# Performance work log

Hardware: AMD Instinct MI355X
Metric: run time of the kernel (lower is better)

## Reference

```python
import jax, jax.numpy as jnp
import numpy as np

B, L, C = 8, 999, 768
C2 = C // 2           # 384 per branch
H, HD = 8, C2 // 8    # heads, head_dim=48
K, G = 3, 2           # dynamic conv kernel size, num_groups
DC_IN = C2 // 4       # DynamicConv1d proj inner (reduction_ratio default 4) = 96
PJ_IN = max(16, C // 8)  # mixer proj inner_dim = 96
SCALE = HD ** -0.5
EPS = 1e-5


def _gelu(x):
    return jax.nn.gelu(x, approximate=False)


def _c1x1(x, w, b):
    # pointwise conv1d: x (B,Cin,L), w (Cout,Cin), b (Cout,)
    return jnp.einsum('bcl,oc->bol', x, w) + b[None, :, None]


def _dw3(x, w, b):
    # depthwise conv1d k=3 pad=1: x (B,Ch,L), w (Ch,3), b (Ch,) or None
    Lx = x.shape[-1]
    xp = jnp.pad(x, ((0, 0), (0, 0), (1, 1)))
    y = (xp[:, :, 0:Lx] * w[:, 0][None, :, None]
         + xp[:, :, 1:Lx + 1] * w[:, 1][None, :, None]
         + xp[:, :, 2:Lx + 2] * w[:, 2][None, :, None])
    if b is not None:
        y = y + b[None, :, None]
    return y


def _bn(x, g, b):
    # BatchNorm1d, training-mode batch stats over (B, L): x (B,Ch,L)
    m = x.mean(axis=(0, 2), keepdims=True)
    v = ((x - m) ** 2).mean(axis=(0, 2), keepdims=True)
    return (x - m) * jax.lax.rsqrt(v + EPS) * g[None, :, None] + b[None, :, None]


def setup_inputs() -> dict:
    key = jax.random.key(0)
    ks = jax.random.split(key, 30)
    s = 0.02
    d = {
        'x': jax.random.normal(ks[0], (B, L, C), jnp.float32),
        # DynamicConv1d (dim=384, K=3, G=2, inner=96)
        'dc_weight': jax.random.normal(ks[1], (G, C2, K), jnp.float32) * s,
        'dc_bias':   jax.random.normal(ks[2], (G, C2), jnp.float32) * s,
        'dc_p1w':    jax.random.normal(ks[3], (DC_IN, C2), jnp.float32) * s,
        'dc_p1b':    jax.random.normal(ks[4], (DC_IN,), jnp.float32) * s,
        'dc_p2w':    jax.random.normal(ks[5], (C2 * G, DC_IN), jnp.float32) * s,
        'dc_p2b':    jax.random.normal(ks[6], (C2 * G,), jnp.float32) * s,
        # Attention (dim=384, heads=8, sr_ratio=1 -> sr=Identity)
        'at_qw':  jax.random.normal(ks[7], (C2, C2), jnp.float32) * s,
        'at_qb':  jax.random.normal(ks[8], (C2,), jnp.float32) * s,
        'at_kvw': jax.random.normal(ks[9], (2 * C2, C2), jnp.float32) * s,
        'at_kvb': jax.random.normal(ks[10], (2 * C2,), jnp.float32) * s,
        'at_lcw': jax.random.normal(ks[11], (C2, K), jnp.float32) * s,
        'at_lcb': jax.random.normal(ks[12], (C2,), jnp.float32) * s,
        # mixer proj
        'pj_dww':  jax.random.normal(ks[13], (C, K), jnp.float32) * s,
        'pj_dwb':  jax.random.normal(ks[14], (C,), jnp.float32) * s,
        'pj_bn1g': jnp.ones((C,), jnp.float32),
        'pj_bn1b': jnp.zeros((C,), jnp.float32),
        'pj_c1w':  jax.random.normal(ks[15], (PJ_IN, C), jnp.float32) * s,
        'pj_c1b':  jax.random.normal(ks[16], (PJ_IN,), jnp.float32) * s,
        'pj_bn2g': jnp.ones((PJ_IN,), jnp.float32),
        'pj_bn2b': jnp.zeros((PJ_IN,), jnp.float32),
        'pj_c2w':  jax.random.normal(ks[17], (C, PJ_IN), jnp.float32) * s,
        'pj_c2b':  jax.random.normal(ks[18], (C,), jnp.float32) * s,
        'pj_bn3g': jnp.ones((C,), jnp.float32),
        'pj_bn3b': jnp.zeros((C,), jnp.float32),
    }
    return d


def _dynamic_conv(x, dc_weight, dc_bias, p1w, p1b, p2w, p2b):
    # x: (B, L, C2)
    xt = jnp.transpose(x, (0, 2, 1))                 # (B,C2,L)
    # AdaptiveAvgPool1d(K) with L divisible by K -> exact non-overlapping mean
    pooled = xt.reshape(B, C2, K, L // K).mean(-1)   # (B,C2,K)
    sc = _c1x1(_gelu(_c1x1(pooled, p1w, p1b)), p2w, p2b)  # (B, G*C2, K)
    sc = jax.nn.softmax(sc.reshape(B, G, C2, K), axis=1)
    w = (sc * dc_weight[None]).sum(axis=1)           # (B,C2,K) per-sample kernels
    xm = xt.mean(axis=2, keepdims=True)              # (B,C2,1)
    sb = _c1x1(_gelu(_c1x1(xm, p1w, p1b)), p2w, p2b) # (B, G*C2, 1)
    sb = jax.nn.softmax(sb.reshape(B, G, C2), axis=1)
    bias = (sb * dc_bias[None]).sum(axis=1)          # (B,C2)
    # depthwise per-(b,c) conv, k=3, pad=1
    xp = jnp.pad(xt, ((0, 0), (0, 0), (1, 1)))
    y = (xp[:, :, 0:L] * w[:, :, 0:1]
         + xp[:, :, 1:L + 1] * w[:, :, 1:2]
         + xp[:, :, 2:L + 2] * w[:, :, 2:3]) + bias[:, :, None]
    return jnp.transpose(y, (0, 2, 1))               # (B,L,C2)


def _attention(x, qw, qb, kvw, kvb, lcw, lcb):
    # x: (B, L, C2)
    xt = jnp.transpose(x, (0, 2, 1))                 # (B,C2,L)
    q = _c1x1(xt, qw, qb).reshape(B, H, HD, L)
    q = jnp.transpose(q, (0, 1, 3, 2))               # (B,H,L,HD)
    kv_in = _dw3(xt, lcw, lcb) + xt                  # local_conv(kv)+kv (sr=Identity)
    kv = _c1x1(kv_in, kvw, kvb)                      # (B,2*C2,L)
    k = kv[:, :C2].reshape(B, H, HD, L)              # (B,H,HD,L)
    v = jnp.transpose(kv[:, C2:].reshape(B, H, HD, L), (0, 1, 3, 2))  # (B,H,L,HD)
    attn = jnp.einsum('bhld,bhdm->bhlm', q, k) * SCALE
    attn = jax.nn.softmax(attn, axis=-1)
    out = jnp.einsum('bhlm,bhmd->bhld', attn, v)     # (B,H,L,HD)
    # faithful to torch: transpose(-1,-2) then reshape(B, L, C2)
    out = jnp.transpose(out, (0, 1, 3, 2)).reshape(B, L, C2)
    return out


def reference(x, dc_weight, dc_bias, dc_p1w, dc_p1b, dc_p2w, dc_p2b,
              at_qw, at_qb, at_kvw, at_kvb, at_lcw, at_lcb,
              pj_dww, pj_dwb, pj_bn1g, pj_bn1b, pj_c1w, pj_c1b,
              pj_bn2g, pj_bn2b, pj_c2w, pj_c2b, pj_bn3g, pj_bn3b):
    x1 = x[:, :, :C2]
    x2 = x[:, :, C2:]
    x1 = _dynamic_conv(x1, dc_weight, dc_bias, dc_p1w, dc_p1b, dc_p2w, dc_p2b)
    x2 = _attention(x2, at_qw, at_qb, at_kvw, at_kvb, at_lcw, at_lcb)
    xc = jnp.concatenate([x1, x2], axis=2)           # (B,L,C)
    xt = jnp.transpose(xc, (0, 2, 1))                # (B,C,L)
    h = _bn(_gelu(_dw3(xt, pj_dww, pj_dwb)), pj_bn1g, pj_bn1b)
    h = _bn(_gelu(_c1x1(h, pj_c1w, pj_c1b)), pj_bn2g, pj_bn2b)
    h = _bn(_c1x1(h, pj_c2w, pj_c2b), pj_bn3g, pj_bn3b)
    out = h + xt
    return jnp.transpose(out, (0, 2, 1))             # (B,L,C)
```

## Files before the change

kernel.cpp:

```cpp
#include <hip/hip_runtime.h>
#include <cstddef>

constexpr int B = 8, L = 999, C = 768, C2 = 384, H = 8, HD = 48;
constexpr int KVL = 1000;
constexpr float ATT_SCALE = 0.14433756729740644f;
constexpr float LOG2E = 1.4426950408889634f;
constexpr float BN_EPS = 1e-5f;
constexpr float INV_N = 1.0f / (8.0f * 999.0f);

constexpr size_t SZ_XT   = (size_t)B * C * L;
constexpr size_t SZ_HALF = (size_t)B * C2 * L;
constexpr size_t OFF_XT  = 0;
constexpr size_t OFF_XT2 = SZ_XT;
constexpr size_t OFF_KV  = 2 * SZ_XT;
constexpr size_t OFF_AX  = 3 * SZ_XT;
constexpr size_t OFF_Q   = 3 * SZ_XT + SZ_HALF;
constexpr size_t OFF_SM  = 3 * SZ_XT + SZ_HALF + SZ_HALF / 2;

constexpr size_t SM_POOLED = 0;
constexpr size_t SM_XM     = 9216;
constexpr size_t SM_H1     = 12288;
constexpr size_t SM_WDYN   = 15360;
constexpr size_t SM_BDYN   = 24576;
constexpr size_t SM_SUM1   = 27648;
constexpr size_t SM_SQ1    = 28416;
constexpr size_t SM_CB1    = 30720;
constexpr size_t SM_SUM2   = 30816;
constexpr size_t SM_SQ2    = 30912;
constexpr size_t SM_CB2    = 31200;
constexpr size_t SM_SUM3   = 31968;
constexpr size_t SM_SQ3    = 32736;
constexpr size_t SM_ZEND   = 33504;
constexpr size_t SM_END    = 35040;
constexpr size_t SM_WQ  = SM_END;
constexpr size_t SM_WKV = SM_WQ + 73728;
constexpr size_t SM_WC1 = SM_WKV + 147456;
constexpr size_t SM_WC2 = SM_WC1 + 36864;

typedef __attribute__((ext_vector_type(8))) short bf16x8;
typedef __attribute__((ext_vector_type(4))) float floatx4;

__device__ __forceinline__ float gelu_f(float x) {
  return 0.5f * x * (1.0f + erff(x * 0.70710678118654752f));
}

__device__ __forceinline__ float wave_sum(float v) {
  #pragma unroll
  for (int off = 32; off > 0; off >>= 1) v += __shfl_down(v, off, 64);
  return v;
}

__device__ __forceinline__ short f2bf(float f) {
  union { float f; unsigned u; } x; x.f = f;
  unsigned r = x.u + 0x7FFFu + ((x.u >> 16) & 1u);
  return (short)(r >> 16);
}

__device__ __forceinline__ bf16x8 pack8(const float* p) {
  union { unsigned u[4]; bf16x8 v; } r;
  asm("v_cvt_pk_bf16_f32 %0, %1, %2" : "=v"(r.u[0]) : "v"(p[0]), "v"(p[1]));
  asm("v_cvt_pk_bf16_f32 %0, %1, %2" : "=v"(r.u[1]) : "v"(p[2]), "v"(p[3]));
  asm("v_cvt_pk_bf16_f32 %0, %1, %2" : "=v"(r.u[2]) : "v"(p[4]), "v"(p[5]));
  asm("v_cvt_pk_bf16_f32 %0, %1, %2" : "=v"(r.u[3]) : "v"(p[6]), "v"(p[7]));
  return r.v;
}

__device__ __forceinline__ float exp2_hw(float x) {
  float r;
  asm("v_exp_f32 %0, %1" : "=v"(r) : "v"(x));
  return r;
}

#define BNA(x, su, qq, gg) { float m_ = (su) * INV_N; float v_ = (qq) * INV_N - m_ * m_; \
  float sc_ = (gg) * rsqrtf(v_ + BN_EPS); (x) = ((x) - m_) * sc_; }

__global__ void k_pre_t(const float* __restrict__ qw, short* __restrict__ wq,
                        const float* __restrict__ kvw, short* __restrict__ wkv,
                        const float* __restrict__ c1w, short* __restrict__ wc1,
                        const float* __restrict__ c2w, short* __restrict__ wc2,
                        const float* __restrict__ c1b, const float* __restrict__ bn1b,
                        const float* __restrict__ c2b, const float* __restrict__ bn2b,
                        float* __restrict__ cb1, float* __restrict__ cb2,
                        const float* __restrict__ x, float* __restrict__ xt) {
  __shared__ float tile[32][33];
  int bid = blockIdx.x;
  int t = threadIdx.y * 32 + threadIdx.x;
  if (bid < 288) {
    const float* src; short* dst; int base;
    if (bid < 72)       { src = qw;  dst = wq;  base = bid; }
    else if (bid < 216) { src = kvw; dst = wkv; base = bid - 72; }
    else if (bid < 252) { src = c1w; dst = wc1; base = bid - 216; }
    else                { src = c2w; dst = wc2; base = bid - 252; }
    int i = (base * 256 + t) * 8;
    float4 a = *reinterpret_cast<const float4*>(&src[i]);
    float4 b = *reinterpret_cast<const float4*>(&src[i + 4]);
    short tmp[8] = {f2bf(a.x), f2bf(a.y), f2bf(a.z), f2bf(a.w),
                    f2bf(b.x), f2bf(b.y), f2bf(b.z), f2bf(b.w)};
    *(bf16x8*)&dst[i] = *(bf16x8*)tmp;
  } else if (bid == 288) {
    if (t < 96) {
      float a = c1b[t];
      const float* wr = c1w + (size_t)t * C;
      for (int c = 0; c < C; c++) a += bn1b[c] * wr[c];
      cb1[t] = a;
    }
  } else if (bid == 289) {
    for (int o = t; o < C; o += 256) {
      float a = c2b[o];
      const float* wr = c2w + (size_t)o * 96;
      for (int i = 0; i < 96; i++) a += bn2b[i] * wr[i];
      cb2[o] = a;
    }
  } else {
    int tb = bid - 290;
    int bx = tb % 32, by = (tb / 32) % 12, bz = tb / 384;
    int l0 = bx * 32, c0 = by * 32;
    int tx = threadIdx.x, ty = threadIdx.y;
    #pragma unroll
    for (int i = 0; i < 4; i++) {
      int l = l0 + ty + i * 8, c = c0 + tx;
      if (l < L) tile[ty + i * 8][tx] = x[((size_t)bz * L + l) * C + c];
    }
    __syncthreads();
    #pragma unroll
    for (int i = 0; i < 4; i++) {
      int c = c0 + ty + i * 8, l = l0 + tx;
      if (l < L) xt[((size_t)bz * C + c) * L + l] = tile[tx][ty + i * 8];
    }
  }
}

__global__ __launch_bounds__(384) void k_kvin(const float* __restrict__ x,
                                              const float* __restrict__ lcw,
                                              const float* __restrict__ lcb,
                                              short* __restrict__ x2bf,
                                              short* __restrict__ kvinbf) {
  int b = blockIdx.y, l0 = blockIdx.x * 8, c = threadIdx.x;
  float w0 = lcw[c * 3], w1 = lcw[c * 3 + 1] + 1.0f, w2 = lcw[c * 3 + 2], bb = lcb[c];
  const float* xb = x + (size_t)b * L * C + C2 + c;
  float prev = (l0 > 0) ? xb[(size_t)(l0 - 1) * C] : 0.f;
  float cur  = (l0 < L) ? xb[(size_t)l0 * C] : 0.f;
  #pragma unroll
  for (int r = 0; r < 8; r++) {
    int l = l0 + r;
    if (l >= L) break;
    float nxt = (l + 1 < L) ? xb[(size_t)(l + 1) * C] : 0.f;
    x2bf[((size_t)b * L + l) * C2 + c]   = f2bf(cur);
    kvinbf[((size_t)b * L + l) * C2 + c] = f2bf(prev * w0 + cur * w1 + nxt * w2 + bb);
    prev = cur; cur = nxt;
  }
}

__global__ __launch_bounds__(256) void k_pool(const float* __restrict__ xt,
                                              float* __restrict__ pooled,
                                              float* __restrict__ xm) {
  int c = blockIdx.x, b = blockIdx.y;
  const float* row = xt + ((size_t)b * C + c) * L;
  float s0 = 0.f, s1 = 0.f, s2 = 0.f;
  for (int l = threadIdx.x; l < L; l += 256) {
    float v = row[l];
    int ch = l / 333;
    if (ch == 0) s0 += v; else if (ch == 1) s1 += v; else s2 += v;
  }
  s0 = wave_sum(s0); s1 = wave_sum(s1); s2 = wave_sum(s2);
  __shared__ float r[3][4];
  int lane = threadIdx.x & 63, wid = threadIdx.x >> 6;
  if (lane == 0) { r[0][wid] = s0; r[1][wid] = s1; r[2][wid] = s2; }
  __syncthreads();
  if (threadIdx.x == 0) {
    float t0 = r[0][0] + r[0][1] + r[0][2] + r[0][3];
    float t1 = r[1][0] + r[1][1] + r[1][2] + r[1][3];
    float t2 = r[2][0] + r[2][1] + r[2][2] + r[2][3];
    size_t pb = (size_t)(b * C2 + c) * 3;
    pooled[pb + 0] = t0 / 333.f;
    pooled[pb + 1] = t1 / 333.f;
    pooled[pb + 2] = t2 / 333.f;
    xm[b * C2 + c] = (t0 + t1 + t2) / 999.f;
  }
}

__global__ void k_mlp1(const float* __restrict__ pooled, const float* __restrict__ xm,
                       const float* __restrict__ p1w, const float* __restrict__ p1b,
                       float* __restrict__ h1) {
  int j = blockIdx.x, b = blockIdx.y;
  __shared__ float vin[C2];
  for (int c = threadIdx.x; c < C2; c += 128)
    vin[c] = (j < 3) ? pooled[(size_t)(b * C2 + c) * 3 + j] : xm[b * C2 + c];
  __syncthreads();
  int o = threadIdx.x;
  if (o < 96) {
    float acc = p1b[o];
    const float* wr = p1w + (size_t)o * C2;
    for (int c = 0; c < C2; c++) acc += vin[c] * wr[c];
    h1[(b * 4 + j) * 96 + o] = gelu_f(acc);
  }
}

__global__ void k_mix2(const float* __restrict__ h1,
                       const float* __restrict__ p2w, const float* __restrict__ p2b,
                       const float* __restrict__ dcw, const float* __restrict__ dcb,
                       float* __restrict__ wdyn, float* __restrict__ bdyn) {
  int j = blockIdx.x, b = blockIdx.y;
  __shared__ float hv[96];
  for (int i = threadIdx.x; i < 96; i += 384) hv[i] = h1[(b * 4 + j) * 96 + i];
  __syncthreads();
  int c = threadIdx.x;
  float a0 = p2b[c], a1 = p2b[C2 + c];
  const float* w0r = p2w + (size_t)c * 96;
  const float* w1r = p2w + (size_t)(C2 + c) * 96;
  for (int i = 0; i < 96; i++) { float h = hv[i]; a0 += h * w0r[i]; a1 += h * w1r[i]; }
  float m = fmaxf(a0, a1);
  float e0 = __expf(a0 - m), e1 = __expf(a1 - m);
  float inv = 1.f / (e0 + e1);
  float p0 = e0 * inv, p1 = e1 * inv;
  if (j < 3)
    wdyn[(size_t)(b * C2 + c) * 3 + j] = p0 * dcw[(size_t)c * 3 + j] + p1 * dcw[(size_t)(C2 + c) * 3 + j];
  else
    bdyn[b * C2 + c] = p0 * dcb[c] + p1 * dcb[C2 + c];
}

__global__ __launch_bounds__(256) void k_dwconv(const float* __restrict__ xt,
                                                const float* __restrict__ wdyn,
                                                const float* __restrict__ bdyn,
                                                float* __restrict__ xt2) {
  int c = blockIdx.x, b = blockIdx.y;
  const float* rowA = xt + ((size_t)b * C + c) * L;
  size_t wb = (size_t)(b * C2 + c) * 3;
  float a0 = wdyn[wb], a1 = wdyn[wb + 1], a2 = wdyn[wb + 2], ab = bdyn[b * C2 + c];
  float* oA = xt2 + ((size_t)b * C + c) * L;
  for (int l = threadIdx.x; l < L; l += 256) {
    float xm1 = (l > 0) ? rowA[l - 1] : 0.f;
    float x0 = rowA[l];
    float xp1 = (l < L - 1) ? rowA[l + 1] : 0.f;
    oA[l] = xm1 * a0 + x0 * a1 + xp1 * a2 + ab;
  }
}

template<int LT, bool XBF16>
__device__ __forceinline__ void gemm_body(const short* __restrict__ Wbf,
                                          const void* __restrict__ Xv,
                                          void* __restrict__ Yv,
                                          const float* __restrict__ ssum,
                                          const float* __restrict__ ssq,
                                          const float* __restrict__ sg,
                                          const float* __restrict__ bias,
                                          float* __restrict__ osum, float* __restrict__ osq,
                                          int O, int Kd, int Kstride, int XLd, int Ldy,
                                          size_t xbs, size_t ybs,
                                          int flags, float outmul,
                                          int kc, size_t slice,
                                          int o0, int l0, int b,
                                          short* Xt) {
  constexpr int R = LT / 32;
  constexpr int XSZ = LT * 72;
  int kbeg = kc * Kd;
  int t = threadIdx.x, w = t >> 6, lane = t & 63;
  int col = lane & 15, quad = lane >> 4;
  int KT = (Kd + 63) >> 6;

  floatx4 acc[LT / 16];
  #pragma unroll
  for (int i = 0; i < LT / 16; i++) acc[i] = floatx4{0.f, 0.f, 0.f, 0.f};

  int orow = o0 + w * 16 + col;
  bool wok = orow < O;
  const short* Wrow = Wbf + (size_t)orow * Kstride + kbeg;

  const short* Xb16 = (const short*)Xv + (size_t)b * xbs + kbeg;
  const float* Xb32 = (const float*)Xv + (size_t)b * xbs + kbeg;

  bf16x8 xr[R];
  float4 xf[R][2];
  bf16x8 wcur0, wcur1, wnxt0, wnxt1;

  auto xload = [&](int k0) {
    #pragma unroll
    for (int r = 0; r < R; r++) {
      int u = t + r * 256;
      int ll = u >> 3, oct = u & 7;
      int l = l0 + ll, kk = k0 + oct * 8;
      bool ok = (l < L) && (kk < Kd);
      if constexpr (XBF16) {
        xr[r] = ok ? *(const bf16x8*)&Xb16[(size_t)l * XLd + kk]
                   : bf16x8{0, 0, 0, 0, 0, 0, 0, 0};
      } else {
        if (ok) {
          const float* p = &Xb32[(size_t)l * XLd + kk];
          float4 a = *(const float4*)p;
          float4 bq = *(const float4*)(p + 4);
          if (sg) {
            float4 u0 = *(const float4*)&ssum[kbeg + kk];
            float4 u1 = *(const float4*)&ssum[kbeg + kk + 4];
            float4 q0 = *(const float4*)&ssq[kbeg + kk];
            float4 q1 = *(const float4*)&ssq[kbeg + kk + 4];
            float4 g0 = *(const float4*)&sg[kbeg + kk];
            float4 g1 = *(const float4*)&sg[kbeg + kk + 4];
            BNA(a.x, u0.x, q0.x, g0.x);  BNA(a.y, u0.y, q0.y, g0.y);
            BNA(a.z, u0.z, q0.z, g0.z);  BNA(a.w, u0.w, q0.w, g0.w);
            BNA(bq.x, u1.x, q1.x, g1.x); BNA(bq.y, u1.y, q1.y, g1.y);
            BNA(bq.z, u1.z, q1.z, g1.z); BNA(bq.w, u1.w, q1.w, g1.w);
          }
          xf[r][0] = a;
          xf[r][1] = bq;
        } else {
          xf[r][0] = float4{0.f, 0.f, 0.f, 0.f};
          xf[r][1] = float4{0.f, 0.f, 0.f, 0.f};
        }
      }
    }
  };
  auto xwrite = [&](int buf) {
    #pragma unroll
    for (int r = 0; r < R; r++) {
      int u = t + r * 256;
      int ll = u >> 3, oct = u & 7;
      bf16x8 val;
      if constexpr (XBF16) {
        val = xr[r];
      } else {
        union { unsigned u4[4]; bf16x8 v; } pk;
        asm("v_cvt_pk_bf16_f32 %0, %1, %2" : "=v"(pk.u4[0]) : "v"(xf[r][0].x), "v"(xf[r][0].y));
        asm("v_cvt_pk_bf16_f32 %0, %1, %2" : "=v"(pk.u4[1]) : "v"(xf[r][0].z), "v"(xf[r][0].w));
        asm("v_cvt_pk_bf16_f32 %0, %1, %2" : "=v"(pk.u4[2]) : "v"(xf[r][1].x), "v"(xf[r][1].y));
        asm("v_cvt_pk_bf16_f32 %0, %1, %2" : "=v"(pk.u4[3]) : "v"(xf[r][1].z), "v"(xf[r][1].w));
        val = pk.v;
      }
      *(bf16x8*)&Xt[buf * XSZ + ll * 72 + oct * 8] = val;
    }
  };
  auto wload = [&](int k0, bf16x8& f0, bf16x8& f1) {
    int kk0 = k0 + quad * 8;
    int kk1 = k0 + 32 + quad * 8;
    f0 = (wok && kk0 < Kd) ? *(const bf16x8*)&Wrow[kk0] : bf16x8{0, 0, 0, 0, 0, 0, 0, 0};
    f1 = (wok && kk1 < Kd) ? *(const bf16x8*)&Wrow[kk1] : bf16x8{0, 0, 0, 0, 0, 0, 0, 0};
  };

  xload(0);
  wload(0, wcur0, wcur1);
  xwrite(0);
  __syncthreads();

  for (int it = 0; it < KT; ++it) {
    int curb = it & 1;
    bool more = (it + 1 < KT);
    if (more) { xload((it + 1) * 64); wload((it + 1) * 64, wnxt0, wnxt1); }
    #pragma unroll
    for (int nt = 0; nt < LT / 16; nt++) {
      bf16x8 bx0 = *(bf16x8*)&Xt[curb * XSZ + (nt * 16 + col) * 72 + quad * 8];
      acc[nt] = __builtin_amdgcn_mfma_f32_16x16x32_bf16(wcur0, bx0, acc[nt], 0, 0, 0);
      bf16x8 bx1 = *(bf16x8*)&Xt[curb * XSZ + (nt * 16 + col) * 72 + 32 + quad * 8];
      acc[nt] = __builtin_amdgcn_mfma_f32_16x16x32_bf16(wcur1, bx1, acc[nt], 0, 0, 0);
    }
    if (more) xwrite(curb ^ 1);
    __syncthreads();
    wcur0 = wnxt0; wcur1 = wnxt1;
  }

  int o_base = o0 + w * 16 + quad * 4;
  #pragma unroll
  for (int r = 0; r < 4; r++) {
    int o = o_base + r;
    bool ov = o < O;
    float bo = (bias && ov) ? bias[o] : 0.f;
    float ps = 0.f, pq = 0.f;
    #pragma unroll
    for (int nt = 0; nt < LT / 16; nt++) {
      int l = l0 + nt * 16 + col;
      float v = acc[nt][r] + bo;
      if (flags & 1) v = gelu_f(v);
      v *= outmul;
      if (l >= L) v = 0.f;
      if (ov && l < L) {
        if (flags & 2) ((short*)Yv)[(size_t)b * ybs + (size_t)o * Ldy + l] = f2bf(v);
        else           ((float*)Yv)[kc * slice + (size_t)b * ybs + (size_t)o * Ldy + l] = v;
      }
      ps += v; pq += v * v;
    }
    if ((flags & 8) && ov) {
      ps += __shfl_xor(ps, 1); ps += __shfl_xor(ps, 2);
      ps += __shfl_xor(ps, 4); ps += __shfl_xor(ps, 8);
      pq += __shfl_xor(pq, 1); pq += __shfl_xor(pq, 2);
      pq += __shfl_xor(pq, 4); pq += __shfl_xor(pq, 8);
      if (col == 0) { atomicAdd(&osum[o], ps); atomicAdd(&osq[o], pq); }
    }
  }
}

template<int LT, bool XBF16>
__global__ __launch_bounds__(256) void k_gemm3(const short* __restrict__ Wbf,
                                               const void* __restrict__ Xv,
                                               void* __restrict__ Yv,
                                               const float* __restrict__ ssum,
                                               const float* __restrict__ ssq,
                                               const float* __restrict__ sg,
                                               const float* __restrict__ bias,
                                               float* __restrict__ osum, float* __restrict__ osq,
                                               int O, int Kd, int Kstride, int XLd, int Ldy,
                                               size_t xbs, size_t ybs,
                                               int flags, float outmul,
                                               int ksplit, size_t slice) {
  __shared__ __align__(16) short Xt[2][LT * 72];
  int kc = (int)blockIdx.y % ksplit;
  int o0 = ((int)blockIdx.y / ksplit) * 64;
  gemm_body<LT, XBF16>(Wbf, Xv, Yv, ssum, ssq, sg, bias, osum, osq,
                       O, Kd, Kstride, XLd, Ldy, xbs, ybs, flags, outmul,
                       kc, slice, o0, blockIdx.x * LT, blockIdx.z, &Xt[0][0]);
}

__global__ __launch_bounds__(256) void k_gemm_qkv(const short* __restrict__ wq,
                                                  const short* __restrict__ wkv,
                                                  const short* __restrict__ x2,
                                                  const short* __restrict__ kvin,
                                                  short* __restrict__ qout,
                                                  short* __restrict__ kvout,
                                                  const float* __restrict__ qbias,
                                                  const float* __restrict__ kvbias) {
  __shared__ __align__(16) short Xt[2][128 * 72];
  int y = blockIdx.y;
  if (y < 6) {
    gemm_body<128, true>(wq, (const void*)x2, (void*)qout,
                         nullptr, nullptr, nullptr, qbias, nullptr, nullptr,
                         C2, C2, C2, C2, L, (size_t)C2 * L, (size_t)C2 * L,
                         2, ATT_SCALE * LOG2E, 0, 0,
                         y * 64, blockIdx.x * 128, blockIdx.z, &Xt[0][0]);
  } else {
    gemm_body<128, true>(wkv, (const void*)kvin, (void*)kvout,
                         nullptr, nullptr, nullptr, kvbias, nullptr, nullptr,
                         C, C2, C2, C2, KVL, (size_t)C2 * L, (size_t)C * KVL,
                         2, 1.0f, 0, 0,
                         (y - 6) * 64, blockIdx.x * 128, blockIdx.z, &Xt[0][0]);
  }
}

__global__ __launch_bounds__(256) void k_h2fin_t(const float* __restrict__ part,
                                                 const float* __restrict__ cb1,
                                                 float* __restrict__ h2,
                                                 float* __restrict__ sum, float* __restrict__ sq) {
  __shared__ float tile[96][33];
  __shared__ float lsum[96], lsq[96];
  constexpr size_t SL = (size_t)B * 96 * L;
  int b = blockIdx.y, l0 = blockIdx.x * 32;
  int t = threadIdx.x;
  #pragma unroll
  for (int p = 0; p < 12; p++) {
    int u = t + p * 256;
    int o = u >> 5, li = u & 31;
    int l = l0 + li;
    float v = 0.f;
    if (l < L) {
      size_t idx = ((size_t)b * 96 + o) * L + l;
      v = gelu_f(part[idx] + part[SL + idx] + part[2 * SL + idx] + part[3 * SL + idx] + cb1[o]);
    }
    tile[o][li] = v;
    float vs = v, vq = v * v;
    vs += __shfl_xor(vs, 1); vs += __shfl_xor(vs, 2); vs += __shfl_xor(vs, 4);
    vs += __shfl_xor(vs, 8); vs += __shfl_xor(vs, 16);
    vq += __shfl_xor(vq, 1); vq += __shfl_xor(vq, 2); vq += __shfl_xor(vq, 4);
    vq += __shfl_xor(vq, 8); vq += __shfl_xor(vq, 16);
    if ((t & 31) == 0) { lsum[o] = vs; lsq[o] = vq; }
  }
  __syncthreads();
  if (t < 96) { atomicAdd(&sum[t], lsum[t]); atomicAdd(&sq[t], lsq[t]); }
  #pragma unroll
  for (int p = 0; p < 12; p++) {
    int u = t + p * 256;
    int lr = u / 96, o = u % 96;
    int l = l0 + lr;
    if (l < L) h2[((size_t)b * L + l) * 96 + o] = tile[o][lr];
  }
}

__global__ __launch_bounds__(512, 4) void k_attn_mfma(const short* __restrict__ q,
                                                      const short* __restrict__ kv,
                                                      float* __restrict__ out) {
  __shared__ __align__(16) char smem[2 * 8192 + 2 * 6144 + 33280];
  short* Ks0 = (short*)smem;
  short* Ks1 = (short*)(smem + 8192);
  short* Vf0 = (short*)(smem + 16384);
  short* Vf1 = (short*)(smem + 22528);
  float* PF  = (float*)(smem + 28672);
  float* Os  = (float*)smem;

  int lt0 = blockIdx.x * 128;
  int h = blockIdx.y, b = blockIdx.z;
  int t = threadIdx.x;
  int w = t >> 6, lane = t & 63;
  int col = lane & 15, quad = lane >> 4;
  const short* qb = q  + ((size_t)b * C2 + h * HD) * L;
  const short* kb = kv + ((size_t)b * C  + h * HD) * KVL;
  const short* vb = kv + ((size_t)b * C + C2 + h * HD) * KVL;

  bf16x8 aq0, aq1;
  {
    int l = lt0 + w * 16 + col;
    bool ok = l < L;
    const short* qp = qb + (size_t)(quad * 8) * L + l;
    short v0[8];
    #pragma unroll
    for (int jj = 0; jj < 8; jj++) v0[jj] = ok ? qp[(size_t)jj * L] : (short)0;
    aq0 = *(bf16x8*)v0;
    if (quad < 2) {
      const short* qp1 = qb + (size_t)(32 + quad * 8) * L + l;
      short v1[8];
      #pragma unroll
      for (int jj = 0; jj < 8; jj++) v1[jj] = ok ? qp1[(size_t)jj * L] : (short)0;
      aq1 = *(bf16x8*)v1;
    } else {
      aq1 = bf16x8{0, 0, 0, 0, 0, 0, 0, 0};
    }
  }

  short kreg[8];
  bf16x8 vreg;

  auto stage_load = [&](int m0) {
    if (t < 384) {
      int m = t & 63, j = t >> 6;
      int gm = m0 + m;
      bool ok = gm < L;
      const short* src = kb + (size_t)(8 * j) * KVL + gm;
      #pragma unroll
      for (int jj = 0; jj < 8; jj++) kreg[jj] = ok ? src[(size_t)jj * KVL] : (short)0;
    }
    if (t >= 128) {
      int a = t - 128;
      int d = (a & 7) | ((a >> 6) << 3);
      int o = (a >> 3) & 7;
      int mb = m0 + o * 8;
      const short* src = vb + (size_t)d * KVL + mb;
      if (mb + 8 <= L) {
        vreg = *(const bf16x8*)src;
      } else {
        short tmp[8];
        #pragma unroll
        for (int j = 0; j < 8; j++) tmp[j] = (mb + j < L) ? src[j] : (short)0;
        vreg = *(bf16x8*)tmp;
      }
    }
  };
  auto stage_write = [&](short* Kd, short* Vd) {
    if (t < 384) {
      int m = t & 63, j = t >> 6;
      int slot = ((m >> 4) * 2 + (j >> 2)) * 64 + (j & 3) * 16 + (m & 15);
      *(bf16x8*)&Kd[slot * 8] = *(bf16x8*)kreg;
    }
    if (t >= 128) {
      int a = t - 128;
      int d = (a & 7) | ((a >> 6) << 3);
      int o = (a >> 3) & 7;
      int lanep = ((o & 3) << 4) | (d & 15);
      *(bf16x8*)&Vd[(((o >> 2) * 3 + (d >> 4)) * 64 + lanep) * 8] = vreg;
    }
  };

  if (t < 256) {
    int i = t & 127;
    int ms = i >> 5, qq = 2 + ((i >> 4) & 1), cc = i & 15;
    int slot = (ms * 2 + 1) * 64 + qq * 16 + cc;
    short* Kd = (t < 128) ? Ks0 : Ks1;
    *(bf16x8*)&Kd[slot * 8] = bf16x8{0, 0, 0, 0, 0, 0, 0, 0};
  }

  stage_load(0);
  stage_write(Ks0, Vf0);

  floatx4 of[3];
  #pragma unroll
  for (int i = 0; i < 3; i++) of[i] = floatx4{0.f, 0.f, 0.f, 0.f};
  float rs[4] = {0.f, 0.f, 0.f, 0.f};
  __syncthreads();

  for (int it = 0; it < 16; ++it) {
    int m0 = it * 64;
    short* Kc = (it & 1) ? Ks1 : Ks0;
    short* Vc = (it & 1) ? Vf1 : Vf0;
    short* Kn = (it & 1) ? Ks0 : Ks1;
    short* Vn = (it & 1) ? Vf0 : Vf1;
    if (it < 15) stage_load(m0 + 64);

    floatx4 sf[4];
    __builtin_amdgcn_s_setprio(1);
    #pragma unroll
    for (int ms = 0; ms < 4; ms++) {
      bf16x8 bk0 = *(bf16x8*)&Kc[((ms * 2 + 0) * 64 + lane) * 8];
      bf16x8 bk1 = *(bf16x8*)&Kc[((ms * 2 + 1) * 64 + lane) * 8];
      floatx4 a4 = floatx4{0.f, 0.f, 0.f, 0.f};
      a4 = __builtin_amdgcn_mfma_f32_16x16x32_bf16(aq0, bk0, a4, 0, 0, 0);
      a4 = __builtin_amdgcn_mfma_f32_16x16x32_bf16(aq1, bk1, a4, 0, 0, 0);
      sf[ms] = a4;
    }
    __builtin_amdgcn_s_setprio(0);

    float* pw = PF + w * 1040 + lane;
    #pragma unroll
    for (int ms = 0; ms < 4; ms++) {
      int m = m0 + ms * 16 + col;
      bool ok = m < L;
      #pragma unroll
      for (int r = 0; r < 4; r++) {
        float e = ok ? exp2_hw(sf[ms][r]) : 0.f;
        rs[r] += e;
        pw[(ms * 4 + r) * 65] = e;
      }
    }

    const float* pr = PF + w * 1040 + (col & 3) * 65 + (col >> 2) * 16 + (quad & 1) * 8;
    __builtin_amdgcn_s_setprio(1);
    #pragma unroll
    for (int mh = 0; mh < 2; mh++) {
      const float* ps = pr + (mh * 2 + (quad >> 1)) * 260;
      float p8[8];
      #pragma unroll
      for (int jj = 0; jj < 8; jj++) p8[jj] = ps[jj];
      bf16x8 ap = pack8(p8);
      #pragma unroll
      for (int ds = 0; ds < 3; ds++) {
        bf16x8 bv = *(bf16x8*)&Vc[((mh * 3 + ds) * 64 + lane) * 8];
        of[ds] = __builtin_amdgcn_mfma_f32_16x16x32_bf16(ap, bv, of[ds], 0, 0, 0);
      }
    }
    __builtin_amdgcn_s_setprio(0);
    if (it < 15) stage_write(Kn, Vn);
    __syncthreads();
  }

  #pragma unroll
  for (int r = 0; r < 4; r++) {
    float v = rs[r];
    v += __shfl_xor(v, 1); v += __shfl_xor(v, 2);
    v += __shfl_xor(v, 4); v += __shfl_xor(v, 8);
    rs[r] = v;
  }
  #pragma unroll
  for (int r = 0; r < 4; r++) {
    float inv = 1.f / rs[r];
    #pragma unroll
    for (int ds = 0; ds < 3; ds++)
      Os[(ds * 16 + col) * 130 + w * 16 + quad * 4 + r] = of[ds][r] * inv;
  }
  __syncthreads();
  for (int i = t; i < 48 * 128; i += 512) {
    int d = i >> 7, ll = i & 127;
    int l = lt0 + ll;
    if (l < L) out[((size_t)b * C2 + h * HD + d) * L + l] = Os[d * 130 + ll];
  }
}

__global__ __launch_bounds__(256) void k_dwproj_t(const float* __restrict__ xt2,
                                                  const float* __restrict__ ao,
                                                  const float* __restrict__ dww,
                                                  const float* __restrict__ dwb,
                                                  float* __restrict__ t1,
                                                  float* __restrict__ sum, float* __restrict__ sq) {
  __shared__ float tile[32][67];
  __shared__ float rs[4][32], rq[4][32];
  int b = blockIdx.z, c0 = blockIdx.y * 32, l0 = blockIdx.x * 64;
  int t = threadIdx.x;
  if (c0 < C2) {
    for (int u = t; u < 32 * 66; u += 256) {
      int cc = u / 66, li = u % 66;
      int l = l0 - 1 + li;
      tile[cc][li] = (l >= 0 && l < L) ? xt2[((size_t)b * C + c0 + cc) * L + l] : 0.f;
    }
  } else {
    for (int u = t; u < 32 * 66; u += 256) {
      int li = u >> 5, cc = u & 31;
      int l = l0 - 1 + li;
      tile[cc][li] = (l >= 0 && l < L) ? ao[((size_t)b * L + l) * C2 + (c0 - C2 + cc)] : 0.f;
    }
  }
  __syncthreads();
  int c = c0 + (t & 31);
  float w0 = dww[c * 3], w1 = dww[c * 3 + 1], w2 = dww[c * 3 + 2], bb = dwb[c];
  int cc = t & 31;
  float s = 0.f, s2 = 0.f;
  #pragma unroll
  for (int p = 0; p < 8; p++) {
    int lr = (t >> 5) + p * 8;
    int l = l0 + lr;
    float v = 0.f;
    if (l < L) {
      v = gelu_f(tile[cc][lr] * w0 + tile[cc][lr + 1] * w1 + tile[cc][lr + 2] * w2 + bb);
      t1[((size_t)b * L + l) * C + c] = v;
    }
    s += v; s2 += v * v;
  }
  s += __shfl_xor(s, 32, 64); s2 += __shfl_xor(s2, 32, 64);
  int wv = t >> 6, ln = t & 63;
  if (ln < 32) { rs[wv][ln] = s; rq[wv][ln] = s2; }
  __syncthreads();
  if (t < 32) {
    float a = rs[0][t] + rs[1][t] + rs[2][t] + rs[3][t];
    float qq = rq[0][t] + rq[1][t] + rq[2][t] + rq[3][t];
    atomicAdd(&sum[c0 + t], a);
    atomicAdd(&sq[c0 + t], qq);
  }
}

__global__ void k_final(const float* __restrict__ y3, const float* __restrict__ xt2,
                        const float* __restrict__ ao,
                        const float* __restrict__ sum3, const float* __restrict__ sq3,
                        const float* __restrict__ bn3g, const float* __restrict__ bn3b,
                        float* __restrict__ out) {
  __shared__ float tile[32][33];
  int b = blockIdx.z;
  int l0 = blockIdx.x * 32, c0 = blockIdx.y * 32;
  int tx = threadIdx.x, ty = threadIdx.y;
  #pragma unroll
  for (int i = 0; i < 4; i++) {
    int c = c0 + ty + i * 8, l = l0 + tx;
    if (l < L) {
      float m = sum3[c] * INV_N;
      float v = sq3[c] * INV_N - m * m;
      float sc = bn3g[c] * rsqrtf(v + BN_EPS);
      float dd = bn3b[c] - m * sc;
      size_t idx = ((size_t)b * C + c) * L + l;
      float val = y3[idx] * sc + dd;
      if (c < C2) val += xt2[idx];
      tile[ty + i * 8][tx] = val;
    }
  }
  __syncthreads();
  #pragma unroll
  for (int i = 0; i < 4; i++) {
    int l = l0 + ty + i * 8, c = c0 + tx;
    if (l < L) {
      float val = tile[tx][ty + i * 8];
      if (c >= C2) val += ao[((size_t)b * L + l) * C2 + (c - C2)];
      out[((size_t)b * L + l) * C + c] = val;
    }
  }
}

extern "C" void kernel_launch(void* const* d_in, const int* in_sizes, int n_in,
                              void* d_out, int out_size, void* d_ws, size_t ws_size,
                              hipStream_t stream) {
  const float* x    = (const float*)d_in[0];
  const float* dcw  = (const float*)d_in[1];
  const float* dcb  = (const float*)d_in[2];
  const float* p1w  = (const float*)d_in[3];
  const float* p1b  = (const float*)d_in[4];
  const float* p2w  = (const float*)d_in[5];
  const float* p2b  = (const float*)d_in[6];
  const float* qw   = (const float*)d_in[7];
  const float* qb   = (const float*)d_in[8];
  const float* kvw  = (const float*)d_in[9];
  const float* kvb  = (const float*)d_in[10];
  const float* lcw  = (const float*)d_in[11];
  const float* lcb  = (const float*)d_in[12];
  const float* dww  = (const float*)d_in[13];
  const float* dwb  = (const float*)d_in[14];
  const float* bn1g = (const float*)d_in[15];
  const float* bn1b = (const float*)d_in[16];
  const float* c1w  = (const float*)d_in[17];
  const float* c1b  = (const float*)d_in[18];
  const float* bn2g = (const float*)d_in[19];
  const float* bn2b = (const float*)d_in[20];
  const float* c2w  = (const float*)d_in[21];
  const float* c2b  = (const float*)d_in[22];
  const float* bn3g = (const float*)d_in[23];
  const float* bn3b = (const float*)d_in[24];
  float* out = (float*)d_out;
  float* ws  = (float*)d_ws;

  float* xt      = ws + OFF_XT;
  float* xt2     = ws + OFF_XT2;
  short* kvbuf   = (short*)(ws + OFF_KV);
  float* c1part  = ws + OFF_KV;
  float* y3      = ws + OFF_KV;
  short* x2bf    = (short*)(ws + OFF_AX);
  short* kvinbf  = (short*)(ws + OFF_AX + SZ_HALF / 2);
  float* attnout = ws + OFF_AX;
  short* qbuf    = (short*)(ws + OFF_Q);
  float* h2      = ws + OFF_Q;
  float* sm      = ws + OFF_SM;

  float* pooled = sm + SM_POOLED;
  float* xm     = sm + SM_XM;
  float* h1     = sm + SM_H1;
  float* wdyn   = sm + SM_WDYN;
  float* bdyn   = sm + SM_BDYN;
  float* sum1 = sm + SM_SUM1; float* sq1 = sm + SM_SQ1;
  float* cb1 = sm + SM_CB1;
  float* sum2 = sm + SM_SUM2; float* sq2 = sm + SM_SQ2;
  float* cb2 = sm + SM_CB2;
  float* sum3 = sm + SM_SUM3; float* sq3 = sm + SM_SQ3;
  short* wqbf  = (short*)(sm + SM_WQ);
  short* wkvbf = (short*)(sm + SM_WKV);
  short* wc1bf = (short*)(sm + SM_WC1);
  short* wc2bf = (short*)(sm + SM_WC2);

  hipMemsetAsync((void*)(sm + SM_SUM1), 0, (SM_ZEND - SM_SUM1) * sizeof(float), stream);

  dim3 tb32(32, 8);
  k_pre_t<<<3362, tb32, 0, stream>>>(qw, wqbf, kvw, wkvbf, c1w, wc1bf, c2w, wc2bf,
                                     c1b, bn1b, c2b, bn2b, cb1, cb2, x, xt);
  k_kvin<<<dim3(125, B), 384, 0, stream>>>(x, lcw, lcb, x2bf, kvinbf);
  k_pool<<<dim3(C2, B), 256, 0, stream>>>(xt, pooled, xm);
  k_mlp1<<<dim3(4, B), 128, 0, stream>>>(pooled, xm, p1w, p1b, h1);
  k_mix2<<<dim3(4, B), 384, 0, stream>>>(h1, p2w, p2b, dcw, dcb, wdyn, bdyn);
  k_dwconv<<<dim3(C2, B), 256, 0, stream>>>(xt, wdyn, bdyn, xt2);
  k_gemm_qkv<<<dim3(8, 18, B), 256, 0, stream>>>(wqbf, wkvbf, x2bf, kvinbf,
                                                 qbuf, kvbuf, qb, kvb);
  k_attn_mfma<<<dim3(8, H, B), 512, 0, stream>>>(qbuf, kvbuf, attnout);
  k_dwproj_t<<<dim3(16, 24, B), 256, 0, stream>>>(xt2, attnout, dww, dwb, xt, sum1, sq1);
  k_gemm3<128, false><<<dim3(8, 8, B), 256, 0, stream>>>(
      wc1bf, (const void*)xt, (void*)c1part, sum1, sq1, bn1g, nullptr, nullptr, nullptr,
      96, 192, C, C, L, (size_t)C * L, (size_t)96 * L, 0, 1.0f, 4, (size_t)B * 96 * L);
  k_h2fin_t<<<dim3(32, B), 256, 0, stream>>>(c1part, cb1, h2, sum2, sq2);
  k_gemm3<128, false><<<dim3(8, 12, B), 256, 0, stream>>>(
      wc2bf, (const void*)h2, (void*)y3, sum2, sq2, bn2g, cb2, sum3, sq3,
      C, 96, 96, 96, L, (size_t)96 * L, (size_t)C * L, 8, 1.0f, 1, 0);
  k_final<<<dim3(32, 24, B), tb32, 0, stream>>>(y3, xt2, attnout, sum3, sq3, bn3g, bn3b, out);
}
```

Baseline: 326.5 us.

## Fuse dynamic-conv MLP kernels and store attention probabilities as bf16

Merges the two small dynamic-conv MLP kernels into one launch, keeping the hidden vector in shared memory instead of a global buffer. In the attention kernel, softmax probabilities are converted to bf16 when written to LDS, so the MFMA A operand is read with one 16-byte load instead of eight float loads plus a pack, and the LDS footprint shrinks. The attention grid is reordered so that batch and head indices vary fastest, which changes block scheduling and cache locality. Rounding to bf16 now happens before the LDS store instead of after, so the numerics stay equivalent.

Result: no change. 321.2 us (-1.6%).

```diff
diff --git a/kernel.cpp b/kernel.cpp
--- a/kernel.cpp
+++ b/kernel.cpp
@@ -19,7 +19,6 @@
 
 constexpr size_t SM_POOLED = 0;
 constexpr size_t SM_XM     = 9216;
-constexpr size_t SM_H1     = 12288;
 constexpr size_t SM_WDYN   = 15360;
 constexpr size_t SM_BDYN   = 24576;
 constexpr size_t SM_SUM1   = 27648;
@@ -54,15 +53,6 @@
   union { float f; unsigned u; } x; x.f = f;
   unsigned r = x.u + 0x7FFFu + ((x.u >> 16) & 1u);
   return (short)(r >> 16);
-}
-
-__device__ __forceinline__ bf16x8 pack8(const float* p) {
-  union { unsigned u[4]; bf16x8 v; } r;
-  asm("v_cvt_pk_bf16_f32 %0, %1, %2" : "=v"(r.u[0]) : "v"(p[0]), "v"(p[1]));
-  asm("v_cvt_pk_bf16_f32 %0, %1, %2" : "=v"(r.u[1]) : "v"(p[2]), "v"(p[3]));
-  asm("v_cvt_pk_bf16_f32 %0, %1, %2" : "=v"(r.u[2]) : "v"(p[4]), "v"(p[5]));
-  asm("v_cvt_pk_bf16_f32 %0, %1, %2" : "=v"(r.u[3]) : "v"(p[6]), "v"(p[7]));
-  return r.v;
 }
 
 __device__ __forceinline__ float exp2_hw(float x) {
@@ -179,32 +169,31 @@
   }
 }
 
-__global__ void k_mlp1(const float* __restrict__ pooled, const float* __restrict__ xm,
-                       const float* __restrict__ p1w, const float* __restrict__ p1b,
-                       float* __restrict__ h1) {
+__global__ __launch_bounds__(384) void k_mlp_mix(const float* __restrict__ pooled,
+                                                 const float* __restrict__ xm,
+                                                 const float* __restrict__ p1w,
+                                                 const float* __restrict__ p1b,
+                                                 const float* __restrict__ p2w,
+                                                 const float* __restrict__ p2b,
+                                                 const float* __restrict__ dcw,
+                                                 const float* __restrict__ dcb,
+                                                 float* __restrict__ wdyn,
+                                                 float* __restrict__ bdyn) {
   int j = blockIdx.x, b = blockIdx.y;
   __shared__ float vin[C2];
-  for (int c = threadIdx.x; c < C2; c += 128)
+  __shared__ float hv[96];
+  int t = threadIdx.x;
+  for (int c = t; c < C2; c += 384)
     vin[c] = (j < 3) ? pooled[(size_t)(b * C2 + c) * 3 + j] : xm[b * C2 + c];
   __syncthreads();
-  int o = threadIdx.x;
-  if (o < 96) {
-    float acc = p1b[o];
-    const float* wr = p1w + (size_t)o * C2;
+  if (t < 96) {
+    float acc = p1b[t];
+    const float* wr = p1w + (size_t)t * C2;
     for (int c = 0; c < C2; c++) acc += vin[c] * wr[c];
-    h1[(b * 4 + j) * 96 + o] = gelu_f(acc);
-  }
-}
-
-__global__ void k_mix2(const float* __restrict__ h1,
-                       const float* __restrict__ p2w, const float* __restrict__ p2b,
-                       const float* __restrict__ dcw, const float* __restrict__ dcb,
-                       float* __restrict__ wdyn, float* __restrict__ bdyn) {
-  int j = blockIdx.x, b = blockIdx.y;
-  __shared__ float hv[96];
-  for (int i = threadIdx.x; i < 96; i += 384) hv[i] = h1[(b * 4 + j) * 96 + i];
-  __syncthreads();
-  int c = threadIdx.x;
+    hv[t] = gelu_f(acc);
+  }
+  __syncthreads();
+  int c = t;
   float a0 = p2b[c], a1 = p2b[C2 + c];
   const float* w0r = p2w + (size_t)c * 96;
   const float* w1r = p2w + (size_t)(C2 + c) * 96;
@@ -473,16 +462,17 @@
 __global__ __launch_bounds__(512, 4) void k_attn_mfma(const short* __restrict__ q,
                                                       const short* __restrict__ kv,
                                                       float* __restrict__ out) {
-  __shared__ __align__(16) char smem[2 * 8192 + 2 * 6144 + 33280];
+  __shared__ __align__(16) char smem[2 * 8192 + 2 * 6144 + 18432];
   short* Ks0 = (short*)smem;
   short* Ks1 = (short*)(smem + 8192);
   short* Vf0 = (short*)(smem + 16384);
   short* Vf1 = (short*)(smem + 22528);
-  float* PF  = (float*)(smem + 28672);
+  short* PFh = (short*)(smem + 28672);
   float* Os  = (float*)smem;
 
-  int lt0 = blockIdx.x * 128;
-  int h = blockIdx.y, b = blockIdx.z;
+  int bh = blockIdx.x;
+  int h = bh & 7, b = bh >> 3;
+  int lt0 = blockIdx.y * 128;
   int t = threadIdx.x;
   int w = t >> 6, lane = t & 63;
   int col = lane & 15, quad = lane >> 4;
@@ -591,7 +581,7 @@
     }
     __builtin_amdgcn_s_setprio(0);
 
-    float* pw = PF + w * 1040 + lane;
+    short* pwh = PFh + w * 1152 + lane;
     #pragma unroll
     for (int ms = 0; ms < 4; ms++) {
       int m = m0 + ms * 16 + col;
@@ -600,19 +590,16 @@
       for (int r = 0; r < 4; r++) {
         float e = ok ? exp2_hw(sf[ms][r]) : 0.f;
         rs[r] += e;
-        pw[(ms * 4 + r) * 65] = e;
+        pwh[(ms * 4 + r) * 72] = f2bf(e);
       }
     }
 
-    const float* pr = PF + w * 1040 + (col & 3) * 65 + (col >> 2) * 16 + (quad & 1) * 8;
     __builtin_amdgcn_s_setprio(1);
     #pragma unroll
     for (int mh = 0; mh < 2; mh++) {
-      const float* ps = pr + (mh * 2 + (quad >> 1)) * 260;
-      float p8[8];
-      #pragma unroll
-      for (int jj = 0; jj < 8; jj++) p8[jj] = ps[jj];
-      bf16x8 ap = pack8(p8);
+      int prow = (col & 3) + 4 * (mh * 2 + (quad >> 1));
+      int pcol = (col >> 2) * 16 + (quad & 1) * 8;
+      bf16x8 ap = *(bf16x8*)&PFh[w * 1152 + prow * 72 + pcol];
       #pragma unroll
       for (int ds = 0; ds < 3; ds++) {
         bf16x8 bv = *(bf16x8*)&Vc[((mh * 3 + ds) * 64 + lane) * 8];
@@ -777,7 +764,6 @@
 
   float* pooled = sm + SM_POOLED;
   float* xm     = sm + SM_XM;
-  float* h1     = sm + SM_H1;
   float* wdyn   = sm + SM_WDYN;
   float* bdyn   = sm + SM_BDYN;
   float* sum1 = sm + SM_SUM1; float* sq1 = sm + SM_SQ1;
@@ -797,12 +783,11 @@
                                      c1b, bn1b, c2b, bn2b, cb1, cb2, x, xt);
   k_kvin<<<dim3(125, B), 384, 0, stream>>>(x, lcw, lcb, x2bf, kvinbf);
   k_pool<<<dim3(C2, B), 256, 0, stream>>>(xt, pooled, xm);
-  k_mlp1<<<dim3(4, B), 128, 0, stream>>>(pooled, xm, p1w, p1b, h1);
-  k_mix2<<<dim3(4, B), 384, 0, stream>>>(h1, p2w, p2b, dcw, dcb, wdyn, bdyn);
+  k_mlp_mix<<<dim3(4, B), 384, 0, stream>>>(pooled, xm, p1w, p1b, p2w, p2b, dcw, dcb, wdyn, bdyn);
   k_dwconv<<<dim3(C2, B), 256, 0, stream>>>(xt, wdyn, bdyn, xt2);
   k_gemm_qkv<<<dim3(8, 18, B), 256, 0, stream>>>(wqbf, wkvbf, x2bf, kvinbf,
                                                  qbuf, kvbuf, qb, kvb);
-  k_attn_mfma<<<dim3(8, H, B), 512, 0, stream>>>(qbuf, kvbuf, attnout);
+  k_attn_mfma<<<dim3(64, 8), 512, 0, stream>>>(qbuf, kvbuf, attnout);
   k_dwproj_t<<<dim3(16, 24, B), 256, 0, stream>>>(xt2, attnout, dww, dwb, xt, sum1, sq1);
   k_gemm3<128, false><<<dim3(8, 8, B), 256, 0, stream>>>(
       wc1bf, (const void*)xt, (void*)c1part, sum1, sq1, bn1g, nullptr, nullptr, nullptr,
```
